# Performance work log

Hardware: AMD Instinct MI355X
Metric: run time of the kernel (lower is better)

Reference implementation:

```python
import jax, jax.numpy as jnp
import numpy as np

N_WIRES = 8
DIM = 2 ** N_WIRES  # 256


def _rx(theta):
    # theta: [] or [N] -> [2,2] or [N,2,2] complex64
    c = jnp.cos(theta / 2)
    s = jnp.sin(theta / 2)
    return jnp.stack([jnp.stack([c + 0j, -1j * s], -1),
                      jnp.stack([-1j * s, c + 0j], -1)], -2)


def _ry(theta):
    c = jnp.cos(theta / 2)
    s = jnp.sin(theta / 2)
    return jnp.stack([jnp.stack([c + 0j, -s + 0j], -1),
                      jnp.stack([s + 0j, c + 0j], -1)], -2)


def _rz(theta):
    e = jnp.exp(-1j * theta / 2)
    z = jnp.zeros_like(e)
    return jnp.stack([jnp.stack([e, z], -1),
                      jnp.stack([z, jnp.conj(e)], -1)], -2)


def _apply_1q(state, U, wire):
    # state: [N, DIM]; U: [2,2] (shared) or [N,2,2] (per-sample)
    s = state.reshape(-1, 2 ** wire, 2, 2 ** (N_WIRES - 1 - wire))
    if U.ndim == 2:
        s = jnp.einsum('ab,nxby->nxay', U, s)
    else:
        s = jnp.einsum('nab,nxby->nxay', U, s)
    return s.reshape(-1, DIM)


def _cnot(state, c, t):
    # wire 0 = most significant bit (PennyLane convention)
    s = state.reshape((-1,) + (2,) * N_WIRES)
    ax_c = 1 + c
    s0 = jnp.take(s, 0, axis=ax_c)
    s1 = jnp.take(s, 1, axis=ax_c)
    ax_t = 1 + t if t < c else t  # target axis after control axis removed
    s1 = jnp.flip(s1, axis=ax_t)
    s = jnp.stack([s0, s1], axis=ax_c)
    return s.reshape(-1, DIM)


def _z_signs():
    idx = np.arange(DIM)
    bits = (idx[:, None] >> (N_WIRES - 1 - np.arange(N_WIRES))[None, :]) & 1
    return jnp.asarray(1.0 - 2.0 * bits, dtype=jnp.float32)  # [DIM, 8]


def _circuit(x_flat, params):
    # x_flat: [N, 8] angles; params: [8, 3]
    n = x_flat.shape[0]
    state = jnp.zeros((n, DIM), dtype=jnp.complex64).at[:, 0].set(1.0)
    for i in range(N_WIRES):
        state = _apply_1q(state, _rx(x_flat[:, i]), i)
    for i in range(N_WIRES):
        state = _apply_1q(state, _ry(params[i, 0]), i)
        state = _apply_1q(state, _rz(params[i, 1]), i)
        state = _apply_1q(state, _rx(params[i, 2]), i)
    for i in range(N_WIRES - 1):
        state = _cnot(state, i, i + 1)
    state = _cnot(state, N_WIRES - 1, 0)
    probs = state.real ** 2 + state.imag ** 2  # [N, DIM]
    return probs @ _z_signs()  # [N, 8] PauliZ expvals


def setup_inputs() -> dict:
    key = jax.random.key(0)
    ks = jax.random.split(key, 4)
    B, S = 16, 2048
    embed_dim, ffn_dim = 512, 2048
    return {
        'x': jax.random.normal(ks[0], (B, S, N_WIRES), dtype=jnp.float32),
        'params': jax.random.normal(ks[1], (N_WIRES, 3), dtype=jnp.float32),
        'W1': jax.random.normal(ks[2], (ffn_dim, N_WIRES), dtype=jnp.float32) * 0.1,
        'b1': jnp.zeros((ffn_dim,), dtype=jnp.float32),
        'W2': jax.random.normal(ks[3], (embed_dim, ffn_dim), dtype=jnp.float32) * 0.02,
        'b2': jnp.zeros((embed_dim,), dtype=jnp.float32),
    }


def reference(x, params, W1, b1, W2, b2):
    B, S, _ = x.shape
    ev = _circuit(x.reshape(-1, N_WIRES), params).reshape(B, S, N_WIRES)
    h = jax.nn.relu(ev @ W1.T + b1)
    return h @ W2.T + b2
```

## Files before the change

kernel.cpp:

```cpp
#include <hip/hip_runtime.h>
#include <hip/hip_bf16.h>

#define NS 32768
#define EMB 512
#define KDIM 2048
#define BM 256
#define BN 128
#define NITER (KDIM / 32)

typedef float f32x16 __attribute__((ext_vector_type(16)));
typedef __bf16 bf16x8 __attribute__((ext_vector_type(8)));
typedef __bf16 bf16x2 __attribute__((ext_vector_type(2)));
typedef unsigned int u32;
typedef unsigned int u32x2 __attribute__((ext_vector_type(2)));
typedef const __attribute__((address_space(1))) u32* gptr_t;
typedef __attribute__((address_space(3))) u32* lptr_t;

#if __has_builtin(__builtin_amdgcn_permlane32_swap)
#define HAS_PLS 1
#else
#define HAS_PLS 0
#endif

__device__ __forceinline__ void gload_lds16(const void* g, void* l) {
    __builtin_amdgcn_global_load_lds((gptr_t)g, (lptr_t)l, 16, 0, 0);
}

__device__ __forceinline__ u32 pkrelu(float lo, float hi) {
    union { bf16x2 h; u32 u; } c;
    c.h[0] = (__bf16)fmaxf(lo, 0.f);
    c.h[1] = (__bf16)fmaxf(hi, 0.f);
    return c.u;
}

__device__ __forceinline__ bf16x8 mk_af(u32 a, u32 b, u32 c, u32 d) {
    union { u32 u[4]; bf16x8 v; } t;
    t.u[0] = a; t.u[1] = b; t.u[2] = c; t.u[3] = d;
    return t.v;
}

__device__ __forceinline__ void h_to_af(const f32x16 h, int lane, int half,
                                        bf16x8& af0, bf16x8& af1) {
    u32 w0  = pkrelu(h[0],  h[1]);  u32 w1v = pkrelu(h[2],  h[3]);
    u32 wA  = pkrelu(h[4],  h[5]);  u32 wB  = pkrelu(h[6],  h[7]);
    u32 w2v = pkrelu(h[8],  h[9]);  u32 w3v = pkrelu(h[10], h[11]);
    u32 wC  = pkrelu(h[12], h[13]); u32 wD  = pkrelu(h[14], h[15]);
#if HAS_PLS
    { u32x2 r = __builtin_amdgcn_permlane32_swap(w0,  wA, false, false); w0  = r[0]; wA = r[1]; }
    { u32x2 r = __builtin_amdgcn_permlane32_swap(w1v, wB, false, false); w1v = r[0]; wB = r[1]; }
    { u32x2 r = __builtin_amdgcn_permlane32_swap(w2v, wC, false, false); w2v = r[0]; wC = r[1]; }
    { u32x2 r = __builtin_amdgcn_permlane32_swap(w3v, wD, false, false); w3v = r[0]; wD = r[1]; }
    af0 = mk_af(w0, w1v, wA, wB);
    af1 = mk_af(w2v, w3v, wC, wD);
#else
    int pl = lane ^ 32;
    u32 pw0 = __shfl((int)w0,  pl), pw1 = __shfl((int)w1v, pl);
    u32 pwA = __shfl((int)wA,  pl), pwB = __shfl((int)wB,  pl);
    u32 pw2 = __shfl((int)w2v, pl), pw3 = __shfl((int)w3v, pl);
    u32 pwC = __shfl((int)wC,  pl), pwD = __shfl((int)wD,  pl);
    af0 = half ? mk_af(pwA, pwB, wA, wB) : mk_af(w0,  w1v, pw0, pw1);
    af1 = half ? mk_af(pwC, pwD, wC, wD) : mk_af(w2v, w3v, pw2, pw3);
#endif
}

__global__ __launch_bounds__(256) void k_prep(const float* __restrict__ W2,
                                              const float* __restrict__ W1,
                                              __hip_bfloat16* __restrict__ W2b,
                                              __hip_bfloat16* __restrict__ W1bg) {
    int t = threadIdx.x;
    if (blockIdx.x < 1024) {
        int i = (blockIdx.x * 256 + t) * 4;
        float4 v = *(const float4*)(W2 + i);
        __hip_bfloat16 o[4];
        o[0] = __float2bfloat16(v.x); o[1] = __float2bfloat16(v.y);
        o[2] = __float2bfloat16(v.z); o[3] = __float2bfloat16(v.w);
        *(ulong1*)(W2b + i) = *(ulong1*)o;
    } else {
        int j = (blockIdx.x - 1024) * 1024 + t * 4;
        float4 w = *(const float4*)(W1 + j);
        __hip_bfloat16 p[4];
        p[0] = __float2bfloat16(w.x); p[1] = __float2bfloat16(w.y);
        p[2] = __float2bfloat16(w.z); p[3] = __float2bfloat16(w.w);
        *(ulong1*)(W1bg + j) = *(ulong1*)p;
    }
}

__global__ __launch_bounds__(256, 2) void k_gemm(
        const float* __restrict__ x,
        const float* __restrict__ params,
        const __hip_bfloat16* __restrict__ W1bg,
        const float* __restrict__ b1,
        const __hip_bfloat16* __restrict__ W2b,
        const float* __restrict__ b2,
        float* __restrict__ C) {
    __shared__ __hip_bfloat16 Bs[2][8 * 512];
    __shared__ __hip_bfloat16 W1s[KDIM * 8];
    __shared__ __hip_bfloat16 b1h[KDIM];
    __shared__ __hip_bfloat16 evs[BM * 8];

    int tid = threadIdx.x, wave = tid >> 6, lane = tid & 63;
    int l31 = lane & 31, half = lane >> 5;
    int bx = blockIdx.x, bm = bx >> 2, bn = bx & 3;

    {
        float K1[8], K2[8];
        #pragma unroll
        for (int i = 0; i < 8; i++) {
            float a = params[i*3+0], b = params[i*3+1], g = params[i*3+2];
            float sa, ca, sb, cb, sg, cg;
            __sincosf(a, &sa, &ca);
            __sincosf(b, &sb, &cb);
            __sincosf(g, &sg, &cg);
            K1[i] = sa*sb*sg + ca*cg;
            K2[i] = cb*sg;
        }
        int n = bm * BM + tid;
        float4 x0 = *(const float4*)(x + (size_t)n*8);
        float4 x1 = *(const float4*)(x + (size_t)n*8 + 4);
        float xs[8] = {x0.x, x0.y, x0.z, x0.w, x1.x, x1.y, x1.z, x1.w};
        float z[8];
        #pragma unroll
        for (int i = 0; i < 8; i++) {
            float s, c;
            __sincosf(xs[i], &s, &c);
            z[i] = c * K1[i] - s * K2[i];
        }
        float evv[8];
        float p = z[0];
        #pragma unroll
        for (int j = 1; j < 8; j++) { p *= z[j]; evv[j] = p; }
        float sfx = z[7];
        #pragma unroll
        for (int j = 6; j >= 1; j--) sfx *= z[j];
        evv[0] = sfx;
        __hip_bfloat16 o[8];
        #pragma unroll
        for (int i = 0; i < 8; i++) o[i] = __float2bfloat16(evv[i]);
        *(bf16x8*)&evs[tid * 8] = *(bf16x8*)o;
    }
    for (int i = tid; i < KDIM; i += 256) {
        *(bf16x8*)&W1s[i * 8] = *(const bf16x8*)(W1bg + (size_t)i * 8);
        b1h[i] = __float2bfloat16(b1[i]);
    }

    const __hip_bfloat16* gBp[2];
    #pragma unroll
    for (int i = 0; i < 2; i++) {
        int f = wave * 2 + i, ni = f >> 1, t = f & 1;
        gBp[i] = W2b + (size_t)(bn*BN + ni*32 + l31) * KDIM + t*16 + half*8;
    }
    #pragma unroll
    for (int i = 0; i < 2; i++) {
        gload_lds16(gBp[i], &Bs[0][(wave*2 + i) * 512]);
        gBp[i] += 32;
    }

    __syncthreads();

    bf16x8 evB0, evB1;
    if (half == 0) {
        evB0 = *(bf16x8*)&evs[(wave * 64 +      l31) * 8];
        evB1 = *(bf16x8*)&evs[(wave * 64 + 32 + l31) * 8];
    } else {
        evB0 = (bf16x8){};
        evB0[0] = (__bf16)1.0f;
        evB1 = evB0;
    }
    const f32x16 z16 = {};

    f32x16 acc[8] = {};

#define COMPUTE_AF(K0, A00, A01, A10, A11) do {                               \
        bf16x8 w1f;                                                           \
        if (half == 0) {                                                      \
            w1f = *(const bf16x8*)&W1s[((K0) + l31) * 8];                     \
        } else {                                                              \
            w1f = (bf16x8){};                                                 \
            w1f[0] = *(const __bf16*)&b1h[(K0) + l31];                        \
        }                                                                     \
        f32x16 h0 = __builtin_amdgcn_mfma_f32_32x32x16_bf16(w1f, evB0, z16, 0, 0, 0); \
        h_to_af(h0, lane, half, A00, A01);                                    \
        f32x16 h1 = __builtin_amdgcn_mfma_f32_32x32x16_bf16(w1f, evB1, z16, 0, 0, 0); \
        h_to_af(h1, lane, half, A10, A11);                                    \
    } while (0)

#define GEMM2_STEP(CB, A00, A01, A10, A11) do {                               \
        __builtin_amdgcn_s_setprio(1);                                        \
        _Pragma("unroll")                                                     \
        for (int ni = 0; ni < 4; ni++) {                                      \
            bf16x8 bf0 = *(bf16x8*)&Bs[CB][(ni*2 + 0) * 512 + lane * 8];      \
            acc[ni]     = __builtin_amdgcn_mfma_f32_32x32x16_bf16(A00, bf0, acc[ni],     0, 0, 0); \
            acc[4 + ni] = __builtin_amdgcn_mfma_f32_32x32x16_bf16(A10, bf0, acc[4 + ni], 0, 0, 0); \
            bf16x8 bf1 = *(bf16x8*)&Bs[CB][(ni*2 + 1) * 512 + lane * 8];      \
            acc[ni]     = __builtin_amdgcn_mfma_f32_32x32x16_bf16(A01, bf1, acc[ni],     0, 0, 0); \
            acc[4 + ni] = __builtin_amdgcn_mfma_f32_32x32x16_bf16(A11, bf1, acc[4 + ni], 0, 0, 0); \
        }                                                                     \
        __builtin_amdgcn_s_setprio(0);                                        \
    } while (0)

    bf16x8 aA00, aA01, aA10, aA11;
    bf16x8 aB00, aB01, aB10, aB11;
    COMPUTE_AF(0, aA00, aA01, aA10, aA11);

    for (int it = 0; it < NITER; it += 2) {
        #pragma unroll
        for (int i = 0; i < 2; i++) {
            gload_lds16(gBp[i], &Bs[1][(wave*2 + i) * 512]);
            gBp[i] += 32;
        }
        COMPUTE_AF((it + 1) * 32, aB00, aB01, aB10, aB11);
        GEMM2_STEP(0, aA00, aA01, aA10, aA11);
        __syncthreads();

        if (it + 2 < NITER) {
            #pragma unroll
            for (int i = 0; i < 2; i++) {
                gload_lds16(gBp[i], &Bs[0][(wave*2 + i) * 512]);
                gBp[i] += 32;
            }
            COMPUTE_AF((it + 2) * 32, aA00, aA01, aA10, aA11);
        }
        GEMM2_STEP(1, aB00, aB01, aB10, aB11);
        __syncthreads();
    }
#undef COMPUTE_AF
#undef GEMM2_STEP

    #pragma unroll
    for (int rg = 0; rg < 2; rg++) {
        int rbase = bm*BM + wave*64 + rg*32 + 4*half;
        #pragma unroll
        for (int ni = 0; ni < 4; ni++) {
            int col = bn*BN + ni*32 + l31;
            float bias = b2[col];
            #pragma unroll
            for (int r = 0; r < 16; r++) {
                int row = rbase + (r & 3) + 8 * (r >> 2);
                C[(size_t)row * EMB + col] = acc[rg*4 + ni][r] + bias;
            }
        }
    }
}

extern "C" void kernel_launch(void* const* d_in, const int* in_sizes, int n_in,
                              void* d_out, int out_size, void* d_ws, size_t ws_size,
                              hipStream_t stream) {
    const float* x      = (const float*)d_in[0];
    const float* params = (const float*)d_in[1];
    const float* W1     = (const float*)d_in[2];
    const float* b1     = (const float*)d_in[3];
    const float* W2     = (const float*)d_in[4];
    const float* b2     = (const float*)d_in[5];
    float* out = (float*)d_out;

    char* ws = (char*)d_ws;
    __hip_bfloat16* W2b  = (__hip_bfloat16*)ws;
    __hip_bfloat16* W1bg = (__hip_bfloat16*)(ws + 2097152);

    k_prep<<<1040, 256, 0, stream>>>(W2, W1, W2b, W1bg);
    k_gemm<<<(NS/BM) * (EMB/BN), 256, 0, stream>>>(x, params, W1bg, b1, W2b, b2, out);
}
```

Measured before the change: 151.0 us.

## Split GEMM block across eight waves and drop cross-lane swaps via W1 row permutation

The block grows from 4 to 8 waves, and each wave now owns 32 rows instead of 64. This halves the per-wave accumulators and h-fragments, and the launch bounds are raised to 512 threads with 4 blocks per SM. The W1/b1 rows are permuted when loaded into LDS, so the MFMA output layout can feed the second GEMM directly without permlane32 swaps or shuffles. In exchange, each W2 tile is loaded once per 32-row wave instead of once per 64 rows, which doubles LDS read traffic per MFMA. Barrier cost also rises with more waves.

```diff
diff --git a/kernel.cpp b/kernel.cpp
--- a/kernel.cpp
+++ b/kernel.cpp
@@ -12,15 +12,8 @@
 typedef __bf16 bf16x8 __attribute__((ext_vector_type(8)));
 typedef __bf16 bf16x2 __attribute__((ext_vector_type(2)));
 typedef unsigned int u32;
-typedef unsigned int u32x2 __attribute__((ext_vector_type(2)));
 typedef const __attribute__((address_space(1))) u32* gptr_t;
 typedef __attribute__((address_space(3))) u32* lptr_t;
-
-#if __has_builtin(__builtin_amdgcn_permlane32_swap)
-#define HAS_PLS 1
-#else
-#define HAS_PLS 0
-#endif
 
 __device__ __forceinline__ void gload_lds16(const void* g, void* l) {
     __builtin_amdgcn_global_load_lds((gptr_t)g, (lptr_t)l, 16, 0, 0);
@@ -39,28 +32,11 @@
     return t.v;
 }
 
-__device__ __forceinline__ void h_to_af(const f32x16 h, int lane, int half,
-                                        bf16x8& af0, bf16x8& af1) {
-    u32 w0  = pkrelu(h[0],  h[1]);  u32 w1v = pkrelu(h[2],  h[3]);
-    u32 wA  = pkrelu(h[4],  h[5]);  u32 wB  = pkrelu(h[6],  h[7]);
-    u32 w2v = pkrelu(h[8],  h[9]);  u32 w3v = pkrelu(h[10], h[11]);
-    u32 wC  = pkrelu(h[12], h[13]); u32 wD  = pkrelu(h[14], h[15]);
-#if HAS_PLS
-    { u32x2 r = __builtin_amdgcn_permlane32_swap(w0,  wA, false, false); w0  = r[0]; wA = r[1]; }
-    { u32x2 r = __builtin_amdgcn_permlane32_swap(w1v, wB, false, false); w1v = r[0]; wB = r[1]; }
-    { u32x2 r = __builtin_amdgcn_permlane32_swap(w2v, wC, false, false); w2v = r[0]; wC = r[1]; }
-    { u32x2 r = __builtin_amdgcn_permlane32_swap(w3v, wD, false, false); w3v = r[0]; wD = r[1]; }
-    af0 = mk_af(w0, w1v, wA, wB);
-    af1 = mk_af(w2v, w3v, wC, wD);
-#else
-    int pl = lane ^ 32;
-    u32 pw0 = __shfl((int)w0,  pl), pw1 = __shfl((int)w1v, pl);
-    u32 pwA = __shfl((int)wA,  pl), pwB = __shfl((int)wB,  pl);
-    u32 pw2 = __shfl((int)w2v, pl), pw3 = __shfl((int)w3v, pl);
-    u32 pwC = __shfl((int)wC,  pl), pwD = __shfl((int)wD,  pl);
-    af0 = half ? mk_af(pwA, pwB, wA, wB) : mk_af(w0,  w1v, pw0, pw1);
-    af1 = half ? mk_af(pwC, pwD, wC, wD) : mk_af(w2v, w3v, pw2, pw3);
-#endif
+__device__ __forceinline__ void h_to_af(const f32x16 h, bf16x8& af0, bf16x8& af1) {
+    af0 = mk_af(pkrelu(h[0], h[1]),  pkrelu(h[2], h[3]),
+                pkrelu(h[4], h[5]),  pkrelu(h[6], h[7]));
+    af1 = mk_af(pkrelu(h[8], h[9]),  pkrelu(h[10], h[11]),
+                pkrelu(h[12], h[13]), pkrelu(h[14], h[15]));
 }
 
 __global__ __launch_bounds__(256) void k_prep(const float* __restrict__ W2,
@@ -85,7 +61,7 @@
     }
 }
 
-__global__ __launch_bounds__(256, 2) void k_gemm(
+__global__ __launch_bounds__(512, 4) void k_gemm(
         const float* __restrict__ x,
         const float* __restrict__ params,
         const __hip_bfloat16* __restrict__ W1bg,
@@ -102,7 +78,7 @@
     int l31 = lane & 31, half = lane >> 5;
     int bx = blockIdx.x, bm = bx >> 2, bn = bx & 3;
 
-    {
+    if (tid < 256) {
         float K1[8], K2[8];
         #pragma unroll
         for (int i = 0; i < 8; i++) {
@@ -138,39 +114,32 @@
         for (int i = 0; i < 8; i++) o[i] = __float2bfloat16(evv[i]);
         *(bf16x8*)&evs[tid * 8] = *(bf16x8*)o;
     }
-    for (int i = tid; i < KDIM; i += 256) {
-        *(bf16x8*)&W1s[i * 8] = *(const bf16x8*)(W1bg + (size_t)i * 8);
-        b1h[i] = __float2bfloat16(b1[i]);
-    }
-
-    const __hip_bfloat16* gBp[2];
-    #pragma unroll
-    for (int i = 0; i < 2; i++) {
-        int f = wave * 2 + i, ni = f >> 1, t = f & 1;
-        gBp[i] = W2b + (size_t)(bn*BN + ni*32 + l31) * KDIM + t*16 + half*8;
-    }
-    #pragma unroll
-    for (int i = 0; i < 2; i++) {
-        gload_lds16(gBp[i], &Bs[0][(wave*2 + i) * 512]);
-        gBp[i] += 32;
-    }
+    for (int i = tid; i < KDIM; i += 512) {
+        int q = (i >> 2) & 3;
+        int src = i + ((q == 1) ? 4 : (q == 2) ? -4 : 0);
+        *(bf16x8*)&W1s[i * 8] = *(const bf16x8*)(W1bg + (size_t)src * 8);
+        b1h[i] = __float2bfloat16(b1[src]);
+    }
+
+    const __hip_bfloat16* gBp =
+        W2b + (size_t)(bn*BN + (wave >> 1)*32 + l31) * KDIM + (wave & 1)*16 + half*8;
+    gload_lds16(gBp, &Bs[0][wave * 512]);
+    gBp += 32;
 
     __syncthreads();
 
-    bf16x8 evB0, evB1;
+    bf16x8 evB;
     if (half == 0) {
-        evB0 = *(bf16x8*)&evs[(wave * 64 +      l31) * 8];
-        evB1 = *(bf16x8*)&evs[(wave * 64 + 32 + l31) * 8];
+        evB = *(bf16x8*)&evs[(wave * 32 + l31) * 8];
     } else {
-        evB0 = (bf16x8){};
-        evB0[0] = (__bf16)1.0f;
-        evB1 = evB0;
+        evB = (bf16x8){};
+        evB[0] = (__bf16)1.0f;
     }
     const f32x16 z16 = {};
 
-    f32x16 acc[8] = {};
-
-#define COMPUTE_AF(K0, A00, A01, A10, A11) do {                               \
+    f32x16 acc[4] = {};
+
+#define COMPUTE_AF(K0, A0, A1) do {                                           \
         bf16x8 w1f;                                                           \
         if (half == 0) {                                                      \
             w1f = *(const bf16x8*)&W1s[((K0) + l31) * 8];                     \
@@ -178,66 +147,53 @@
             w1f = (bf16x8){};                                                 \
             w1f[0] = *(const __bf16*)&b1h[(K0) + l31];                        \
         }                                                                     \
-        f32x16 h0 = __builtin_amdgcn_mfma_f32_32x32x16_bf16(w1f, evB0, z16, 0, 0, 0); \
-        h_to_af(h0, lane, half, A00, A01);                                    \
-        f32x16 h1 = __builtin_amdgcn_mfma_f32_32x32x16_bf16(w1f, evB1, z16, 0, 0, 0); \
-        h_to_af(h1, lane, half, A10, A11);                                    \
+        f32x16 h = __builtin_amdgcn_mfma_f32_32x32x16_bf16(w1f, evB, z16, 0, 0, 0); \
+        h_to_af(h, A0, A1);                                                   \
     } while (0)
 
-#define GEMM2_STEP(CB, A00, A01, A10, A11) do {                               \
+#define GEMM2_STEP(CB, A0, A1) do {                                           \
         __builtin_amdgcn_s_setprio(1);                                        \
         _Pragma("unroll")                                                     \
         for (int ni = 0; ni < 4; ni++) {                                      \
             bf16x8 bf0 = *(bf16x8*)&Bs[CB][(ni*2 + 0) * 512 + lane * 8];      \
-            acc[ni]     = __builtin_amdgcn_mfma_f32_32x32x16_bf16(A00, bf0, acc[ni],     0, 0, 0); \
-            acc[4 + ni] = __builtin_amdgcn_mfma_f32_32x32x16_bf16(A10, bf0, acc[4 + ni], 0, 0, 0); \
+            acc[ni] = __builtin_amdgcn_mfma_f32_32x32x16_bf16(A0, bf0, acc[ni], 0, 0, 0); \
             bf16x8 bf1 = *(bf16x8*)&Bs[CB][(ni*2 + 1) * 512 + lane * 8];      \
-            acc[ni]     = __builtin_amdgcn_mfma_f32_32x32x16_bf16(A01, bf1, acc[ni],     0, 0, 0); \
-            acc[4 + ni] = __builtin_amdgcn_mfma_f32_32x32x16_bf16(A11, bf1, acc[4 + ni], 0, 0, 0); \
+            acc[ni] = __builtin_amdgcn_mfma_f32_32x32x16_bf16(A1, bf1, acc[ni], 0, 0, 0); \
         }                                                                     \
         __builtin_amdgcn_s_setprio(0);                                        \
     } while (0)
 
-    bf16x8 aA00, aA01, aA10, aA11;
-    bf16x8 aB00, aB01, aB10, aB11;
-    COMPUTE_AF(0, aA00, aA01, aA10, aA11);
+    bf16x8 aA0, aA1;
+    bf16x8 aB0, aB1;
+    COMPUTE_AF(0, aA0, aA1);
 
     for (int it = 0; it < NITER; it += 2) {
-        #pragma unroll
-        for (int i = 0; i < 2; i++) {
-            gload_lds16(gBp[i], &Bs[1][(wave*2 + i) * 512]);
-            gBp[i] += 32;
-        }
-        COMPUTE_AF((it + 1) * 32, aB00, aB01, aB10, aB11);
-        GEMM2_STEP(0, aA00, aA01, aA10, aA11);
+        gload_lds16(gBp, &Bs[1][wave * 512]);
+        gBp += 32;
+        COMPUTE_AF((it + 1) * 32, aB0, aB1);
+        GEMM2_STEP(0, aA0, aA1);
         __syncthreads();
 
         if (it + 2 < NITER) {
-            #pragma unroll
-            for (int i = 0; i < 2; i++) {
-                gload_lds16(gBp[i], &Bs[0][(wave*2 + i) * 512]);
-                gBp[i] += 32;
-            }
-            COMPUTE_AF((it + 2) * 32, aA00, aA01, aA10, aA11);
-        }
-        GEMM2_STEP(1, aB00, aB01, aB10, aB11);
+            gload_lds16(gBp, &Bs[0][wave * 512]);
+            gBp += 32;
+            COMPUTE_AF((it + 2) * 32, aA0, aA1);
+        }
+        GEMM2_STEP(1, aB0, aB1);
         __syncthreads();
     }
 #undef COMPUTE_AF
 #undef GEMM2_STEP
 
+    int rbase = bm*BM + wave*32 + 4*half;
     #pragma unroll
-    for (int rg = 0; rg < 2; rg++) {
-        int rbase = bm*BM + wave*64 + rg*32 + 4*half;
-        #pragma unroll
-        for (int ni = 0; ni < 4; ni++) {
-            int col = bn*BN + ni*32 + l31;
-            float bias = b2[col];
-            #pragma unroll
-            for (int r = 0; r < 16; r++) {
-                int row = rbase + (r & 3) + 8 * (r >> 2);
-                C[(size_t)row * EMB + col] = acc[rg*4 + ni][r] + bias;
-            }
+    for (int ni = 0; ni < 4; ni++) {
+        int col = bn*BN + ni*32 + l31;
+        float bias = b2[col];
+        #pragma unroll
+        for (int r = 0; r < 16; r++) {
+            int row = rbase + (r & 3) + 8 * (r >> 2);
+            C[(size_t)row * EMB + col] = acc[ni][r] + bias;
         }
     }
 }
@@ -258,5 +214,5 @@
     __hip_bfloat16* W1bg = (__hip_bfloat16*)(ws + 2097152);
 
     k_prep<<<1040, 256, 0, stream>>>(W2, W1, W2b, W1bg);
-    k_gemm<<<(NS/BM) * (EMB/BN), 256, 0, stream>>>(x, params, W1bg, b1, W2b, b2, out);
-}
+    k_gemm<<<(NS/BM) * (EMB/BN), 512, 0, stream>>>(x, params, W1bg, b1, W2b, b2, out);
+}
```

Result: no change. 150.6 us (-0.2%).

## Use 4-stage LDS ring with vmcnt waits and drop permlane swap via W1 row permutation

Applied to the files above, without the earlier changes.

Replaces the double-buffered W2 tile staging with a four-buffer ring that keeps two loads in flight. Each iteration now waits on an explicit vmcnt and issues a single barrier, instead of two full __syncthreads per pair of steps. It also permutes the W1 and b1 rows when staging them into LDS, so the MFMA output layout already matches the A-fragment layout. That removes the permlane32 swaps/shuffles in the ReLU-to-bf16 conversion. The cost is extra LDS, which may reduce occupancy, and correctness now depends on the row permutation and vmcnt accounting being exactly right.

```diff
diff --git a/kernel.cpp b/kernel.cpp
--- a/kernel.cpp
+++ b/kernel.cpp
@@ -12,15 +12,8 @@
 typedef __bf16 bf16x8 __attribute__((ext_vector_type(8)));
 typedef __bf16 bf16x2 __attribute__((ext_vector_type(2)));
 typedef unsigned int u32;
-typedef unsigned int u32x2 __attribute__((ext_vector_type(2)));
 typedef const __attribute__((address_space(1))) u32* gptr_t;
 typedef __attribute__((address_space(3))) u32* lptr_t;
-
-#if __has_builtin(__builtin_amdgcn_permlane32_swap)
-#define HAS_PLS 1
-#else
-#define HAS_PLS 0
-#endif
 
 __device__ __forceinline__ void gload_lds16(const void* g, void* l) {
     __builtin_amdgcn_global_load_lds((gptr_t)g, (lptr_t)l, 16, 0, 0);
@@ -39,28 +32,11 @@
     return t.v;
 }
 
-__device__ __forceinline__ void h_to_af(const f32x16 h, int lane, int half,
-                                        bf16x8& af0, bf16x8& af1) {
-    u32 w0  = pkrelu(h[0],  h[1]);  u32 w1v = pkrelu(h[2],  h[3]);
-    u32 wA  = pkrelu(h[4],  h[5]);  u32 wB  = pkrelu(h[6],  h[7]);
-    u32 w2v = pkrelu(h[8],  h[9]);  u32 w3v = pkrelu(h[10], h[11]);
-    u32 wC  = pkrelu(h[12], h[13]); u32 wD  = pkrelu(h[14], h[15]);
-#if HAS_PLS
-    { u32x2 r = __builtin_amdgcn_permlane32_swap(w0,  wA, false, false); w0  = r[0]; wA = r[1]; }
-    { u32x2 r = __builtin_amdgcn_permlane32_swap(w1v, wB, false, false); w1v = r[0]; wB = r[1]; }
-    { u32x2 r = __builtin_amdgcn_permlane32_swap(w2v, wC, false, false); w2v = r[0]; wC = r[1]; }
-    { u32x2 r = __builtin_amdgcn_permlane32_swap(w3v, wD, false, false); w3v = r[0]; wD = r[1]; }
-    af0 = mk_af(w0, w1v, wA, wB);
-    af1 = mk_af(w2v, w3v, wC, wD);
-#else
-    int pl = lane ^ 32;
-    u32 pw0 = __shfl((int)w0,  pl), pw1 = __shfl((int)w1v, pl);
-    u32 pwA = __shfl((int)wA,  pl), pwB = __shfl((int)wB,  pl);
-    u32 pw2 = __shfl((int)w2v, pl), pw3 = __shfl((int)w3v, pl);
-    u32 pwC = __shfl((int)wC,  pl), pwD = __shfl((int)wD,  pl);
-    af0 = half ? mk_af(pwA, pwB, wA, wB) : mk_af(w0,  w1v, pw0, pw1);
-    af1 = half ? mk_af(pwC, pwD, wC, wD) : mk_af(w2v, w3v, pw2, pw3);
-#endif
+__device__ __forceinline__ void h_to_af(const f32x16 h, bf16x8& af0, bf16x8& af1) {
+    af0 = mk_af(pkrelu(h[0], h[1]),  pkrelu(h[2], h[3]),
+                pkrelu(h[4], h[5]),  pkrelu(h[6], h[7]));
+    af1 = mk_af(pkrelu(h[8], h[9]),  pkrelu(h[10], h[11]),
+                pkrelu(h[12], h[13]), pkrelu(h[14], h[15]));
 }
 
 __global__ __launch_bounds__(256) void k_prep(const float* __restrict__ W2,
@@ -93,7 +69,7 @@
         const __hip_bfloat16* __restrict__ W2b,
         const float* __restrict__ b2,
         float* __restrict__ C) {
-    __shared__ __hip_bfloat16 Bs[2][8 * 512];
+    __shared__ __hip_bfloat16 Bs[4][8 * 512];
     __shared__ __hip_bfloat16 W1s[KDIM * 8];
     __shared__ __hip_bfloat16 b1h[KDIM];
     __shared__ __hip_bfloat16 evs[BM * 8];
@@ -139,8 +115,10 @@
         *(bf16x8*)&evs[tid * 8] = *(bf16x8*)o;
     }
     for (int i = tid; i < KDIM; i += 256) {
-        *(bf16x8*)&W1s[i * 8] = *(const bf16x8*)(W1bg + (size_t)i * 8);
-        b1h[i] = __float2bfloat16(b1[i]);
+        int q = (i >> 2) & 3;
+        int src = i + ((q == 1) ? 4 : (q == 2) ? -4 : 0);
+        *(bf16x8*)&W1s[i * 8] = *(const bf16x8*)(W1bg + (size_t)src * 8);
+        b1h[i] = __float2bfloat16(b1[src]);
     }
 
     const __hip_bfloat16* gBp[2];
@@ -150,9 +128,12 @@
         gBp[i] = W2b + (size_t)(bn*BN + ni*32 + l31) * KDIM + t*16 + half*8;
     }
     #pragma unroll
-    for (int i = 0; i < 2; i++) {
-        gload_lds16(gBp[i], &Bs[0][(wave*2 + i) * 512]);
-        gBp[i] += 32;
+    for (int b = 0; b < 2; b++) {
+        #pragma unroll
+        for (int i = 0; i < 2; i++) {
+            gload_lds16(gBp[i], &Bs[b][(wave*2 + i) * 512]);
+            gBp[i] += 32;
+        }
     }
 
     __syncthreads();
@@ -179,9 +160,9 @@
             w1f[0] = *(const __bf16*)&b1h[(K0) + l31];                        \
         }                                                                     \
         f32x16 h0 = __builtin_amdgcn_mfma_f32_32x32x16_bf16(w1f, evB0, z16, 0, 0, 0); \
-        h_to_af(h0, lane, half, A00, A01);                                    \
+        h_to_af(h0, A00, A01);                                                \
         f32x16 h1 = __builtin_amdgcn_mfma_f32_32x32x16_bf16(w1f, evB1, z16, 0, 0, 0); \
-        h_to_af(h1, lane, half, A10, A11);                                    \
+        h_to_af(h1, A10, A11);                                                \
     } while (0)
 
 #define GEMM2_STEP(CB, A00, A01, A10, A11) do {                               \
@@ -198,31 +179,32 @@
         __builtin_amdgcn_s_setprio(0);                                        \
     } while (0)
 
+#define K_ITER(T, BUF, DO_STAGE, VMC) do {                                    \
+        if (DO_STAGE) {                                                       \
+            gload_lds16(gBp[0], &Bs[((BUF) + 2) & 3][(wave*2 + 0) * 512]);    \
+            gload_lds16(gBp[1], &Bs[((BUF) + 2) & 3][(wave*2 + 1) * 512]);    \
+            gBp[0] += 32; gBp[1] += 32;                                       \
+        }                                                                     \
+        COMPUTE_AF((T) * 32, aA00, aA01, aA10, aA11);                         \
+        asm volatile("s_waitcnt vmcnt(" VMC ")" ::: "memory");                \
+        __builtin_amdgcn_s_barrier();                                         \
+        GEMM2_STEP(BUF, aA00, aA01, aA10, aA11);                              \
+    } while (0)
+
     bf16x8 aA00, aA01, aA10, aA11;
-    bf16x8 aB00, aB01, aB10, aB11;
-    COMPUTE_AF(0, aA00, aA01, aA10, aA11);
-
-    for (int it = 0; it < NITER; it += 2) {
-        #pragma unroll
-        for (int i = 0; i < 2; i++) {
-            gload_lds16(gBp[i], &Bs[1][(wave*2 + i) * 512]);
-            gBp[i] += 32;
-        }
-        COMPUTE_AF((it + 1) * 32, aB00, aB01, aB10, aB11);
-        GEMM2_STEP(0, aA00, aA01, aA10, aA11);
-        __syncthreads();
-
-        if (it + 2 < NITER) {
-            #pragma unroll
-            for (int i = 0; i < 2; i++) {
-                gload_lds16(gBp[i], &Bs[0][(wave*2 + i) * 512]);
-                gBp[i] += 32;
-            }
-            COMPUTE_AF((it + 2) * 32, aA00, aA01, aA10, aA11);
-        }
-        GEMM2_STEP(1, aB00, aB01, aB10, aB11);
-        __syncthreads();
-    }
+
+    for (int it0 = 0; it0 < NITER - 4; it0 += 4) {
+        K_ITER(it0 + 0, 0, 1, "4");
+        K_ITER(it0 + 1, 1, 1, "4");
+        K_ITER(it0 + 2, 2, 1, "4");
+        K_ITER(it0 + 3, 3, 1, "4");
+    }
+    K_ITER(NITER - 4, 0, 1, "4");
+    K_ITER(NITER - 3, 1, 1, "4");
+    K_ITER(NITER - 2, 2, 0, "2");
+    K_ITER(NITER - 1, 3, 0, "0");
+
+#undef K_ITER
 #undef COMPUTE_AF
 #undef GEMM2_STEP
 
```

Result: faster. 147.9 us, median of 2 (-2.0%).
